# Performance work log

Measured on AMD Instinct MI355X. Metric: run time of the kernel, lower is better.

Reference implementation:

```python
import jax, jax.numpy as jnp
import numpy as np

F_SIZE = 1000   # feature_size
FIELDS = 39     # field_size
K = 40          # ffm embedding dim
BATCH = 4096
LAYERS = [1024, 512, 256]


def setup_inputs() -> dict:
    key = jax.random.key(0)
    ks = jax.random.split(key, 12)
    inp = {
        "X": jax.random.normal(ks[0], (BATCH, F_SIZE), dtype=jnp.float32),
        "w1": jax.random.normal(ks[1], (F_SIZE,), dtype=jnp.float32) * 0.01,
        "b": jnp.full((1,), 0.5, dtype=jnp.float32),
        "nfk": jax.random.normal(ks[2], (F_SIZE, FIELDS, K), dtype=jnp.float32) * 0.01,
        "f2f": jax.random.randint(ks[3], (F_SIZE,), 0, FIELDS, dtype=jnp.int32),
    }
    dims = [F_SIZE] + LAYERS
    for i in range(len(LAYERS)):
        fan_in, fan_out = dims[i], dims[i + 1]
        scale = np.sqrt(6.0 / (fan_in + fan_out)).astype(np.float32)
        inp[f"deepW{i}"] = jax.random.uniform(ks[4 + i], (fan_in, fan_out), dtype=jnp.float32, minval=-scale, maxval=scale)
        inp[f"deepB{i}"] = jnp.zeros((fan_out,), dtype=jnp.float32)
    scale = np.sqrt(6.0 / (LAYERS[-1] + 1)).astype(np.float32)
    inp["outW"] = jax.random.uniform(ks[10], (LAYERS[-1], 1), dtype=jnp.float32, minval=-scale, maxval=scale)
    inp["outB"] = jnp.zeros((1,), dtype=jnp.float32)
    return inp


def reference(X, w1, b, nfk, f2f, deepW0, deepB0, deepW1, deepB1, deepW2, deepB2, outW, outB):
    # --- linear term: sum_i w1[i]*X[:,i] + b ---
    linear = X @ w1 + b[0]                                  # [B]

    # --- field-aware interaction ---
    # A[i, j, :] = nfk[i, f2f[j], :]  (gather over fields)
    F = nfk.shape[0]
    A = nfk[jnp.arange(F)[:, None], f2f[None, :], :]        # [F, F, K]
    # S[i, j] = <nfk[i, f2f[j]], nfk[j, f2f[i]]> -- batch-independent scalar
    S = jnp.einsum('ijk,jik->ij', A, A)                     # [F, F]
    M = jnp.triu(S, 1)                                      # keep i < j pairs only
    # sum_{i<j} S[i,j] * X[:,i] * X[:,j]
    interaction = jnp.sum((X @ M) * X, axis=1)              # [B]

    # --- deep part (train=False: no dropout) ---
    h = jax.nn.relu(X @ deepW0 + deepB0)
    h = jax.nn.relu(h @ deepW1 + deepB1)
    h = jax.nn.relu(h @ deepW2 + deepB2)
    deep = (h @ outW + outB).reshape(-1)                    # [B]

    out_sum = linear + interaction + deep                   # logits [B]
    return out_sum
```

## Files before the change

### kernel.cpp

```cpp
#include <hip/hip_runtime.h>


#define BATCH   4096
#define FSZ     1000
#define NFIELDS 39
#define KDIM    40

typedef __attribute__((ext_vector_type(8))) short short8v;
typedef __attribute__((ext_vector_type(4))) float f32x4;

__device__ __forceinline__ short f2bf(float f) {
  unsigned u = __builtin_bit_cast(unsigned, f);
  u += 0x7fff + ((u >> 16) & 1);
  return (short)(u >> 16);
}
__device__ __forceinline__ float bf2f(unsigned short h) {
  unsigned u = (unsigned)h << 16;
  return __builtin_bit_cast(float, u);
}

typedef const __attribute__((address_space(1))) unsigned int* gas_ptr;
typedef __attribute__((address_space(3))) unsigned int* las_ptr;
__device__ __forceinline__ void gload16(const void* g, void* l) {
  __builtin_amdgcn_global_load_lds((gas_ptr)g, (las_ptr)l, 16, 0, 0);
}

__device__ __forceinline__ void transp32(
    const float* __restrict__ in, short* __restrict__ out, int idx, int nx,
    int K_in, int N_in, int Kpad, float (*t)[33], int tid)
{
  int n0 = (idx % nx) * 32, k0 = (idx / nx) * 32;
  int tx = tid & 31, ty = tid >> 5;
  #pragma unroll
  for (int i = 0; i < 32; i += 8) {
    int k = k0 + ty + i, n = n0 + tx;
    t[ty + i][tx] = (k < K_in && n < N_in) ? in[(size_t)k * N_in + n] : 0.f;
  }
  __syncthreads();
  #pragma unroll
  for (int i = 0; i < 32; i += 8) {
    int n = n0 + ty + i, k = k0 + tx;
    if (n < N_in && k < Kpad) out[(size_t)n * Kpad + k] = f2bf(t[tx][ty + i]);
  }
}

__global__ __launch_bounds__(256) void prep_kernel(
    const float* __restrict__ X, const float* __restrict__ nfk,
    const int* __restrict__ f2f,
    const float* __restrict__ W0, const float* __restrict__ W1,
    const float* __restrict__ W2,
    short* __restrict__ Xb, short* __restrict__ B12,
    short* __restrict__ Wt1, short* __restrict__ Wt2)
{
  __shared__ float tbuf[32][33];
  __shared__ float C[NFIELDS * 44];
  const int bid = blockIdx.x, tid = threadIdx.x;
  if (bid < 4096) {
    int k = tid * 4;
    short4 o = make_short4(0, 0, 0, 0);
    if (k < FSZ) {
      float4 v = *(const float4*)(X + (size_t)bid * FSZ + k);
      o = make_short4(f2bf(v.x), f2bf(v.y), f2bf(v.z), f2bf(v.w));
    }
    *(short4*)(Xb + (size_t)bid * 1024 + k) = o;
  } else if (bid < 5120) {
    int n = bid - 4096;
    if (n < FSZ) {
      for (int t = tid; t < NFIELDS * KDIM; t += 256)
        C[(t / KDIM) * 44 + (t % KDIM)] = nfk[(size_t)n * (NFIELDS * KDIM) + t];
    }
    __syncthreads();
    int fn = (n < FSZ) ? f2f[n] : 0;
    #pragma unroll
    for (int kk = 0; kk < 4; ++kk) {
      int k = kk * 256 + tid;
      float s = 0.f;
      if (n < FSZ && k < n) {
        int fk = f2f[k];
        const float4* p = (const float4*)(nfk + ((size_t)k * NFIELDS + fn) * KDIM);
        const float4* q = (const float4*)&C[fk * 44];
        #pragma unroll
        for (int t = 0; t < KDIM / 4; ++t) {
          float4 a = p[t], b = q[t];
          s += a.x * b.x + a.y * b.y + a.z * b.z + a.w * b.w;
        }
      }
      B12[(size_t)n * 1024 + k] = f2bf(s);
    }
  } else if (bid < 6144) {
    transp32(W0, B12 + 1024 * 1024, bid - 5120, 32, 1000, 1024, 1024, tbuf, tid);
  } else if (bid < 6656) {
    transp32(W1, Wt1, bid - 6144, 16, 1024, 512, 1024, tbuf, tid);
  } else {
    transp32(W2, Wt2, bid - 6656, 8, 512, 256, 512, tbuf, tid);
  }
}

template<int BM, int BN, int EPI>
__global__ __launch_bounds__(256) void gemm_mfma(
    const short* __restrict__ A, const short* __restrict__ Bt,
    const float* __restrict__ bias, void* __restrict__ Cout,
    int N, int K,
    const short* __restrict__ Xb, const float* __restrict__ w1,
    float* __restrict__ partial,
    const float* __restrict__ c1, const float* __restrict__ c2)
{
  constexpr int AM = BM / 32, AN = BN / 32;
  __shared__ __align__(16) short As[2][BM * 64];
  __shared__ __align__(16) short Bs[2][BN * 64];
  __shared__ float pbuf[2][BM];

  const int tid  = threadIdx.x;
  const int wid  = tid >> 6;
  const int lane = tid & 63;
  const int wr   = wid >> 1, wc = wid & 1;
  const int row0 = blockIdx.y * BM;
  const int col0 = blockIdx.x * BN;

  const int lr8   = lane >> 3;
  const int cbase = (lane & 7) * 16;

  f32x4 acc[AM][AN];
  #pragma unroll
  for (int m = 0; m < AM; ++m)
    #pragma unroll
    for (int n = 0; n < AN; ++n) acc[m][n] = (f32x4)(0.f);

  auto stage = [&](int p, int k0) {
    #pragma unroll
    for (int j = 0; j < BM / 32; ++j) {
      int i = j * 4 + wid;
      int r = i * 8 + lr8;
      int cb = cbase ^ ((r & 7) << 4);
      gload16((const char*)A + (((size_t)(row0 + r) * K + k0) << 1) + cb,
              (char*)&As[p][0] + i * 1024);
    }
    #pragma unroll
    for (int j = 0; j < BN / 32; ++j) {
      int i = j * 4 + wid;
      int r = i * 8 + lr8;
      int cb = cbase ^ ((r & 7) << 4);
      gload16((const char*)Bt + (((size_t)(col0 + r) * K + k0) << 1) + cb,
              (char*)&Bs[p][0] + i * 1024);
    }
  };

  auto compute = [&](int p) {
    #pragma unroll
    for (int kk = 0; kk < 2; ++kk) {
      const int cb = kk * 64 + (lane >> 4) * 16;
      short8v a[AM], b[AN];
      #pragma unroll
      for (int m = 0; m < AM; ++m) {
        int r = wr * (BM / 2) + m * 16 + (lane & 15);
        a[m] = *(const short8v*)((const char*)&As[p][0] + r * 128 + (cb ^ ((r & 7) << 4)));
      }
      #pragma unroll
      for (int n = 0; n < AN; ++n) {
        int r = wc * (BN / 2) + n * 16 + (lane & 15);
        b[n] = *(const short8v*)((const char*)&Bs[p][0] + r * 128 + (cb ^ ((r & 7) << 4)));
      }
      #pragma unroll
      for (int m = 0; m < AM; ++m)
        #pragma unroll
        for (int n = 0; n < AN; ++n)
          acc[m][n] = __builtin_amdgcn_mfma_f32_16x16x32_bf16(a[m], b[n], acc[m][n], 0, 0, 0);
    }
  };

  int nt = K >> 6;
  if (EPI == 0 && blockIdx.x < 8) {
    int need = ((int)blockIdx.x * 2) + 2;
    nt = nt < need ? nt : need;
  }

  stage(0, 0);
  __syncthreads();
  for (int t = 0; t < nt; ++t) {
    if (t + 1 < nt) stage((t + 1) & 1, (t + 1) << 6);
    compute(t & 1);
    __syncthreads();
  }

  const int cr = (lane >> 4) * 4;
  const int cc = lane & 15;

  if (EPI == 0) {
    if (blockIdx.x < 8) {
      float rsum[AM * 4];
      #pragma unroll
      for (int i = 0; i < AM * 4; ++i) rsum[i] = 0.f;
      #pragma unroll
      for (int m = 0; m < AM; ++m) {
        #pragma unroll
        for (int n = 0; n < AN; ++n) {
          int gc = col0 + wc * (BN / 2) + n * 16 + cc;
          float w1v = (gc < FSZ) ? w1[gc] : 0.f;
          #pragma unroll
          for (int r = 0; r < 4; ++r) {
            int gr = row0 + wr * (BM / 2) + m * 16 + cr + r;
            float xv = bf2f((unsigned short)Xb[(size_t)gr * 1024 + gc]);
            rsum[m * 4 + r] = fmaf(acc[m][n][r] + w1v, xv, rsum[m * 4 + r]);
          }
        }
      }
      #pragma unroll
      for (int mask = 1; mask < 16; mask <<= 1)
        #pragma unroll
        for (int i = 0; i < AM * 4; ++i)
          rsum[i] += __shfl_xor(rsum[i], mask, 64);
      if (cc == 0) {
        #pragma unroll
        for (int m = 0; m < AM; ++m)
          #pragma unroll
          for (int r = 0; r < 4; ++r)
            pbuf[wc][wr * (BM / 2) + m * 16 + cr + r] = rsum[m * 4 + r];
      }
      __syncthreads();
      if (tid < BM)
        partial[(size_t)(row0 + tid) * 8 + blockIdx.x] = pbuf[0][tid] + pbuf[1][tid];
    } else {
      #pragma unroll
      for (int m = 0; m < AM; ++m) {
        #pragma unroll
        for (int n = 0; n < AN; ++n) {
          int gc = col0 - 1024 + wc * (BN / 2) + n * 16 + cc;
          float bv = bias[gc];
          #pragma unroll
          for (int r = 0; r < 4; ++r) {
            int gr = row0 + wr * (BM / 2) + m * 16 + cr + r;
            float v = fmaxf(acc[m][n][r] + bv, 0.f);
            ((short*)Cout)[(size_t)gr * 1024 + gc] = f2bf(v);
          }
        }
      }
    }
  } else if (EPI == 1) {
    #pragma unroll
    for (int m = 0; m < AM; ++m) {
      #pragma unroll
      for (int n = 0; n < AN; ++n) {
        int gc = col0 + wc * (BN / 2) + n * 16 + cc;
        float bv = bias[gc];
        #pragma unroll
        for (int r = 0; r < 4; ++r) {
          int gr = row0 + wr * (BM / 2) + m * 16 + cr + r;
          float v = fmaxf(acc[m][n][r] + bv, 0.f);
          ((short*)Cout)[(size_t)gr * N + gc] = f2bf(v);
        }
      }
    }
  } else {
    float rsum[AM * 4];
    #pragma unroll
    for (int i = 0; i < AM * 4; ++i) rsum[i] = 0.f;
    #pragma unroll
    for (int m = 0; m < AM; ++m) {
      #pragma unroll
      for (int n = 0; n < AN; ++n) {
        int gc = col0 + wc * (BN / 2) + n * 16 + cc;
        float bv = bias[gc];
        float ow = w1[gc];
        #pragma unroll
        for (int r = 0; r < 4; ++r) {
          float v = fmaxf(acc[m][n][r] + bv, 0.f);
          rsum[m * 4 + r] = fmaf(v, ow, rsum[m * 4 + r]);
        }
      }
    }
    #pragma unroll
    for (int mask = 1; mask < 16; mask <<= 1)
      #pragma unroll
      for (int i = 0; i < AM * 4; ++i)
        rsum[i] += __shfl_xor(rsum[i], mask, 64);
    if (cc == 0) {
      #pragma unroll
      for (int m = 0; m < AM; ++m)
        #pragma unroll
        for (int r = 0; r < 4; ++r)
          pbuf[wc][wr * (BM / 2) + m * 16 + cr + r] = rsum[m * 4 + r];
    }
    __syncthreads();
    if (tid < BM) {
      int gr = row0 + tid;
      const float4* pp = (const float4*)(partial + (size_t)gr * 8);
      float4 u = pp[0], v = pp[1];
      ((float*)Cout)[gr] = pbuf[0][tid] + pbuf[1][tid]
          + u.x + u.y + u.z + u.w + v.x + v.y + v.z + v.w + c1[0] + c2[0];
    }
  }
}

extern "C" void kernel_launch(void* const* d_in, const int* in_sizes, int n_in,
                              void* d_out, int out_size, void* d_ws, size_t ws_size,
                              hipStream_t stream) {
  const float* X   = (const float*)d_in[0];
  const float* w1  = (const float*)d_in[1];
  const float* bsc = (const float*)d_in[2];
  const float* nfk = (const float*)d_in[3];
  const int*   f2f = (const int*)d_in[4];
  const float* W0  = (const float*)d_in[5];
  const float* B0  = (const float*)d_in[6];
  const float* W1  = (const float*)d_in[7];
  const float* B1  = (const float*)d_in[8];
  const float* W2  = (const float*)d_in[9];
  const float* B2  = (const float*)d_in[10];
  const float* oW  = (const float*)d_in[11];
  const float* oB  = (const float*)d_in[12];
  float* out = (float*)d_out;

  char* ws = (char*)d_ws;
  short* Xb   = (short*)(ws);
  short* B12  = (short*)(ws + 8388608);
  short* Wt1  = (short*)(ws + 12582912);
  short* Wt2  = (short*)(ws + 13631488);
  float* part = (float*)(ws + 13893632);
  short* h0   = (short*)(ws + 14680064);
  short* h1   = (short*)(ws + 23068672);

  prep_kernel<<<6784, 256, 0, stream>>>(X, nfk, f2f, W0, W1, W2,
                                        Xb, B12, Wt1, Wt2);
  gemm_mfma<128, 128, 0><<<dim3(16, 32), 256, 0, stream>>>(
      Xb, B12, B0, h0, 2048, 1024, Xb, w1, part, nullptr, nullptr);
  gemm_mfma<64, 64, 1><<<dim3(8, 64), 256, 0, stream>>>(
      h0, Wt1, B1, h1, 512, 1024, nullptr, nullptr, nullptr, nullptr, nullptr);
  gemm_mfma<32, 256, 3><<<dim3(1, 128), 256, 0, stream>>>(
      h1, Wt2, B2, out, 256, 512, nullptr, oW, part, bsc, oB);
}
```

Measured before the change: 77.89 us.

## Fuse prep and three GEMMs into one cooperative persistent kernel with grid syncs

Replaces four kernel launches with a single cooperative kernel of 512 blocks that strides over the prep work units, then runs each GEMM stage separated by grid-wide barriers, reusing one 64KB shared buffer. The last GEMM switches to single-buffered staging so its shared footprint fits. The aim is to remove launch gaps and inter-kernel drain between stages. The costs are grid-sync overhead, only 512 resident blocks doing the 6784 prep units, reduced occupancy from the 64KB static shared memory, and a serialized final stage. Falls back to the original launches if the cooperative launch fails.

```diff
diff --git a/kernel.cpp b/kernel.cpp
--- a/kernel.cpp
+++ b/kernel.cpp
@@ -1,4 +1,6 @@
 #include <hip/hip_runtime.h>
+#include <hip/hip_cooperative_groups.h>
+namespace cg = cooperative_groups;
 
 
 #define BATCH   4096
@@ -44,7 +46,8 @@
   }
 }
 
-__global__ __launch_bounds__(256) void prep_kernel(
+__device__ __forceinline__ void prep_unit(
+    int u, int tid, char* sm,
     const float* __restrict__ X, const float* __restrict__ nfk,
     const int* __restrict__ f2f,
     const float* __restrict__ W0, const float* __restrict__ W1,
@@ -52,19 +55,18 @@
     short* __restrict__ Xb, short* __restrict__ B12,
     short* __restrict__ Wt1, short* __restrict__ Wt2)
 {
-  __shared__ float tbuf[32][33];
-  __shared__ float C[NFIELDS * 44];
-  const int bid = blockIdx.x, tid = threadIdx.x;
-  if (bid < 4096) {
+  float (*tbuf)[33] = (float(*)[33])sm;
+  float* C = (float*)(sm + 4224);
+  if (u < 4096) {
     int k = tid * 4;
     short4 o = make_short4(0, 0, 0, 0);
     if (k < FSZ) {
-      float4 v = *(const float4*)(X + (size_t)bid * FSZ + k);
+      float4 v = *(const float4*)(X + (size_t)u * FSZ + k);
       o = make_short4(f2bf(v.x), f2bf(v.y), f2bf(v.z), f2bf(v.w));
     }
-    *(short4*)(Xb + (size_t)bid * 1024 + k) = o;
-  } else if (bid < 5120) {
-    int n = bid - 4096;
+    *(short4*)(Xb + (size_t)u * 1024 + k) = o;
+  } else if (u < 5120) {
+    int n = u - 4096;
     if (n < FSZ) {
       for (int t = tid; t < NFIELDS * KDIM; t += 256)
         C[(t / KDIM) * 44 + (t % KDIM)] = nfk[(size_t)n * (NFIELDS * KDIM) + t];
@@ -87,17 +89,18 @@
       }
       B12[(size_t)n * 1024 + k] = f2bf(s);
     }
-  } else if (bid < 6144) {
-    transp32(W0, B12 + 1024 * 1024, bid - 5120, 32, 1000, 1024, 1024, tbuf, tid);
-  } else if (bid < 6656) {
-    transp32(W1, Wt1, bid - 6144, 16, 1024, 512, 1024, tbuf, tid);
+  } else if (u < 6144) {
+    transp32(W0, B12 + 1024 * 1024, u - 5120, 32, 1000, 1024, 1024, tbuf, tid);
+  } else if (u < 6656) {
+    transp32(W1, Wt1, u - 6144, 16, 1024, 512, 1024, tbuf, tid);
   } else {
-    transp32(W2, Wt2, bid - 6656, 8, 512, 256, 512, tbuf, tid);
+    transp32(W2, Wt2, u - 6656, 8, 512, 256, 512, tbuf, tid);
   }
 }
 
 template<int BM, int BN, int EPI>
-__global__ __launch_bounds__(256) void gemm_mfma(
+__device__ __forceinline__ void gemm_body(
+    char* sm, int bx, int by,
     const short* __restrict__ A, const short* __restrict__ Bt,
     const float* __restrict__ bias, void* __restrict__ Cout,
     int N, int K,
@@ -106,17 +109,19 @@
     const float* __restrict__ c1, const float* __restrict__ c2)
 {
   constexpr int AM = BM / 32, AN = BN / 32;
-  __shared__ __align__(16) short As[2][BM * 64];
-  __shared__ __align__(16) short Bs[2][BN * 64];
-  __shared__ float pbuf[2][BM];
+  constexpr bool DB = (EPI != 3);
+  constexpr int ABUF = 128 * BM;
+  constexpr int BBUF = 128 * BN;
+  char* Asb = sm;
+  char* Bsb = sm + (DB ? 2 * ABUF : ABUF);
+  float (*pb)[BM] = (float(*)[BM])sm;
 
   const int tid  = threadIdx.x;
   const int wid  = tid >> 6;
   const int lane = tid & 63;
   const int wr   = wid >> 1, wc = wid & 1;
-  const int row0 = blockIdx.y * BM;
-  const int col0 = blockIdx.x * BN;
-
+  const int row0 = by * BM;
+  const int col0 = bx * BN;
   const int lr8   = lane >> 3;
   const int cbase = (lane & 7) * 16;
 
@@ -133,7 +138,7 @@
       int r = i * 8 + lr8;
       int cb = cbase ^ ((r & 7) << 4);
       gload16((const char*)A + (((size_t)(row0 + r) * K + k0) << 1) + cb,
-              (char*)&As[p][0] + i * 1024);
+              Asb + p * ABUF + i * 1024);
     }
     #pragma unroll
     for (int j = 0; j < BN / 32; ++j) {
@@ -141,7 +146,7 @@
       int r = i * 8 + lr8;
       int cb = cbase ^ ((r & 7) << 4);
       gload16((const char*)Bt + (((size_t)(col0 + r) * K + k0) << 1) + cb,
-              (char*)&Bs[p][0] + i * 1024);
+              Bsb + p * BBUF + i * 1024);
     }
   };
 
@@ -153,12 +158,12 @@
       #pragma unroll
       for (int m = 0; m < AM; ++m) {
         int r = wr * (BM / 2) + m * 16 + (lane & 15);
-        a[m] = *(const short8v*)((const char*)&As[p][0] + r * 128 + (cb ^ ((r & 7) << 4)));
+        a[m] = *(const short8v*)(Asb + p * ABUF + r * 128 + (cb ^ ((r & 7) << 4)));
       }
       #pragma unroll
       for (int n = 0; n < AN; ++n) {
         int r = wc * (BN / 2) + n * 16 + (lane & 15);
-        b[n] = *(const short8v*)((const char*)&Bs[p][0] + r * 128 + (cb ^ ((r & 7) << 4)));
+        b[n] = *(const short8v*)(Bsb + p * BBUF + r * 128 + (cb ^ ((r & 7) << 4)));
       }
       #pragma unroll
       for (int m = 0; m < AM; ++m)
@@ -169,16 +174,27 @@
   };
 
   int nt = K >> 6;
-  if (EPI == 0 && blockIdx.x < 8) {
-    int need = ((int)blockIdx.x * 2) + 2;
+  if (EPI == 0 && bx < 8) {
+    int need = bx * 2 + 2;
     nt = nt < need ? nt : need;
   }
 
-  stage(0, 0);
-  __syncthreads();
-  for (int t = 0; t < nt; ++t) {
-    if (t + 1 < nt) stage((t + 1) & 1, (t + 1) << 6);
-    compute(t & 1);
+  if constexpr (DB) {
+    stage(0, 0);
+    __syncthreads();
+    for (int t = 0; t < nt; ++t) {
+      if (t + 1 < nt) stage((t + 1) & 1, (t + 1) << 6);
+      compute(t & 1);
+      __syncthreads();
+    }
+  } else {
+    for (int t = 0; t < nt; ++t) {
+      __syncthreads();
+      stage(0, t << 6);
+      asm volatile("s_waitcnt vmcnt(0)" ::: "memory");
+      __syncthreads();
+      compute(0);
+    }
     __syncthreads();
   }
 
@@ -186,7 +202,7 @@
   const int cc = lane & 15;
 
   if (EPI == 0) {
-    if (blockIdx.x < 8) {
+    if (bx < 8) {
       float rsum[AM * 4];
       #pragma unroll
       for (int i = 0; i < AM * 4; ++i) rsum[i] = 0.f;
@@ -214,11 +230,11 @@
         for (int m = 0; m < AM; ++m)
           #pragma unroll
           for (int r = 0; r < 4; ++r)
-            pbuf[wc][wr * (BM / 2) + m * 16 + cr + r] = rsum[m * 4 + r];
+            pb[wc][wr * (BM / 2) + m * 16 + cr + r] = rsum[m * 4 + r];
       }
       __syncthreads();
       if (tid < BM)
-        partial[(size_t)(row0 + tid) * 8 + blockIdx.x] = pbuf[0][tid] + pbuf[1][tid];
+        partial[(size_t)(row0 + tid) * 8 + bx] = pb[0][tid] + pb[1][tid];
     } else {
       #pragma unroll
       for (int m = 0; m < AM; ++m) {
@@ -278,17 +294,67 @@
       for (int m = 0; m < AM; ++m)
         #pragma unroll
         for (int r = 0; r < 4; ++r)
-          pbuf[wc][wr * (BM / 2) + m * 16 + cr + r] = rsum[m * 4 + r];
+          pb[wc][wr * (BM / 2) + m * 16 + cr + r] = rsum[m * 4 + r];
     }
     __syncthreads();
     if (tid < BM) {
       int gr = row0 + tid;
       const float4* pp = (const float4*)(partial + (size_t)gr * 8);
       float4 u = pp[0], v = pp[1];
-      ((float*)Cout)[gr] = pbuf[0][tid] + pbuf[1][tid]
+      ((float*)Cout)[gr] = pb[0][tid] + pb[1][tid]
           + u.x + u.y + u.z + u.w + v.x + v.y + v.z + v.w + c1[0] + c2[0];
     }
   }
+}
+
+__global__ __launch_bounds__(256, 2) void fused_kernel(
+    const float* X, const float* w1, const float* bsc, const float* nfk,
+    const int* f2f, const float* W0, const float* B0, const float* W1,
+    const float* B1, const float* W2, const float* B2, const float* oW,
+    const float* oB, float* out,
+    short* Xb, short* B12, short* Wt1, short* Wt2,
+    float* part, short* h0, short* h1)
+{
+  __shared__ __align__(16) char smem[65536];
+  cg::grid_group grid = cg::this_grid();
+  const int bid = blockIdx.x, tid = threadIdx.x;
+
+  for (int u = bid; u < 6784; u += 512) {
+    prep_unit(u, tid, smem, X, nfk, f2f, W0, W1, W2, Xb, B12, Wt1, Wt2);
+    __syncthreads();
+  }
+  grid.sync();
+  gemm_body<128, 128, 0>(smem, bid & 15, bid >> 4, Xb, B12, B0, h0,
+                         2048, 1024, Xb, w1, part, nullptr, nullptr);
+  grid.sync();
+  gemm_body<64, 64, 1>(smem, bid & 7, bid >> 3, h0, Wt1, B1, h1,
+                       512, 1024, nullptr, nullptr, nullptr, nullptr, nullptr);
+  grid.sync();
+  if (bid < 128)
+    gemm_body<32, 256, 3>(smem, 0, bid, h1, Wt2, B2, out,
+                          256, 512, nullptr, oW, part, bsc, oB);
+}
+
+__global__ __launch_bounds__(256) void prep_kernel(
+    const float* X, const float* nfk, const int* f2f,
+    const float* W0, const float* W1, const float* W2,
+    short* Xb, short* B12, short* Wt1, short* Wt2)
+{
+  __shared__ __align__(16) char smem[11136];
+  prep_unit(blockIdx.x, threadIdx.x, smem, X, nfk, f2f, W0, W1, W2,
+            Xb, B12, Wt1, Wt2);
+}
+
+template<int BM, int BN, int EPI>
+__global__ __launch_bounds__(256) void gemm_mfma(
+    const short* A, const short* Bt, const float* bias, void* Cout,
+    int N, int K, const short* Xb, const float* w1, float* partial,
+    const float* c1, const float* c2)
+{
+  constexpr int SM = (EPI != 3) ? 256 * (BM + BN) : 128 * (BM + BN);
+  __shared__ __align__(16) char smem[SM];
+  gemm_body<BM, BN, EPI>(smem, blockIdx.x, blockIdx.y, A, Bt, bias, Cout,
+                         N, K, Xb, w1, partial, c1, c2);
 }
 
 extern "C" void kernel_launch(void* const* d_in, const int* in_sizes, int n_in,
@@ -318,12 +384,24 @@
   short* h0   = (short*)(ws + 14680064);
   short* h1   = (short*)(ws + 23068672);
 
-  prep_kernel<<<6784, 256, 0, stream>>>(X, nfk, f2f, W0, W1, W2,
-                                        Xb, B12, Wt1, Wt2);
-  gemm_mfma<128, 128, 0><<<dim3(16, 32), 256, 0, stream>>>(
-      Xb, B12, B0, h0, 2048, 1024, Xb, w1, part, nullptr, nullptr);
-  gemm_mfma<64, 64, 1><<<dim3(8, 64), 256, 0, stream>>>(
-      h0, Wt1, B1, h1, 512, 1024, nullptr, nullptr, nullptr, nullptr, nullptr);
-  gemm_mfma<32, 256, 3><<<dim3(1, 128), 256, 0, stream>>>(
-      h1, Wt2, B2, out, 256, 512, nullptr, oW, part, bsc, oB);
-}
+  void* args[] = {
+    (void*)&X, (void*)&w1, (void*)&bsc, (void*)&nfk, (void*)&f2f,
+    (void*)&W0, (void*)&B0, (void*)&W1, (void*)&B1, (void*)&W2, (void*)&B2,
+    (void*)&oW, (void*)&oB, (void*)&out,
+    (void*)&Xb, (void*)&B12, (void*)&Wt1, (void*)&Wt2,
+    (void*)&part, (void*)&h0, (void*)&h1 };
+
+  hipError_t err = hipLaunchCooperativeKernel(
+      (const void*)fused_kernel, dim3(512), dim3(256), args, 0, stream);
+
+  if (err != hipSuccess) {
+    prep_kernel<<<6784, 256, 0, stream>>>(X, nfk, f2f, W0, W1, W2,
+                                          Xb, B12, Wt1, Wt2);
+    gemm_mfma<128, 128, 0><<<dim3(16, 32), 256, 0, stream>>>(
+        Xb, B12, B0, h0, 2048, 1024, Xb, w1, part, nullptr, nullptr);
+    gemm_mfma<64, 64, 1><<<dim3(8, 64), 256, 0, stream>>>(
+        h0, Wt1, B1, h1, 512, 1024, nullptr, nullptr, nullptr, nullptr, nullptr);
+    gemm_mfma<32, 256, 3><<<dim3(1, 128), 256, 0, stream>>>(
+        h1, Wt2, B2, out, 256, 512, nullptr, oW, part, bsc, oB);
+  }
+}
```

Measured after the change: 265.6 us. 3.41x slower.

## Split prep kernel with field-major nfk copy and XCD-aware GEMM block swizzle

Applied to the files above, without the earlier changes.

The S-matrix computation is moved to a separate kernel that reads from a new field-major copy of nfk (nfkT[g][j][k]). With that layout, threads handling consecutive k load contiguous 160-byte rows instead of rows strided by 39*40 floats. The copy is built by extra blocks in the first prep kernel, which costs one more launch and roughly 6 MB of extra traffic. Separately, the GEMM kernels remap block indices so that blocks landing on the same XCD (lin&7) cover contiguous tiles, aiming for better L2 reuse.

```diff
diff --git a/kernel.cpp b/kernel.cpp
--- a/kernel.cpp
+++ b/kernel.cpp
@@ -44,16 +44,15 @@
   }
 }
 
-__global__ __launch_bounds__(256) void prep_kernel(
+__global__ __launch_bounds__(256) void prep_a_kernel(
     const float* __restrict__ X, const float* __restrict__ nfk,
-    const int* __restrict__ f2f,
     const float* __restrict__ W0, const float* __restrict__ W1,
     const float* __restrict__ W2,
     short* __restrict__ Xb, short* __restrict__ B12,
-    short* __restrict__ Wt1, short* __restrict__ Wt2)
+    short* __restrict__ Wt1, short* __restrict__ Wt2,
+    float* __restrict__ nfkT)
 {
   __shared__ float tbuf[32][33];
-  __shared__ float C[NFIELDS * 44];
   const int bid = blockIdx.x, tid = threadIdx.x;
   if (bid < 4096) {
     int k = tid * 4;
@@ -64,35 +63,52 @@
     }
     *(short4*)(Xb + (size_t)bid * 1024 + k) = o;
   } else if (bid < 5120) {
-    int n = bid - 4096;
-    if (n < FSZ) {
-      for (int t = tid; t < NFIELDS * KDIM; t += 256)
-        C[(t / KDIM) * 44 + (t % KDIM)] = nfk[(size_t)n * (NFIELDS * KDIM) + t];
-    }
-    __syncthreads();
-    int fn = (n < FSZ) ? f2f[n] : 0;
-    #pragma unroll
-    for (int kk = 0; kk < 4; ++kk) {
-      int k = kk * 256 + tid;
-      float s = 0.f;
-      if (n < FSZ && k < n) {
-        int fk = f2f[k];
-        const float4* p = (const float4*)(nfk + ((size_t)k * NFIELDS + fn) * KDIM);
-        const float4* q = (const float4*)&C[fk * 44];
-        #pragma unroll
-        for (int t = 0; t < KDIM / 4; ++t) {
-          float4 a = p[t], b = q[t];
-          s += a.x * b.x + a.y * b.y + a.z * b.z + a.w * b.w;
-        }
-      }
-      B12[(size_t)n * 1024 + k] = f2bf(s);
-    }
-  } else if (bid < 6144) {
-    transp32(W0, B12 + 1024 * 1024, bid - 5120, 32, 1000, 1024, 1024, tbuf, tid);
-  } else if (bid < 6656) {
-    transp32(W1, Wt1, bid - 6144, 16, 1024, 512, 1024, tbuf, tid);
+    transp32(W0, B12 + 1024 * 1024, bid - 4096, 32, 1000, 1024, 1024, tbuf, tid);
+  } else if (bid < 5632) {
+    transp32(W1, Wt1, bid - 5120, 16, 1024, 512, 1024, tbuf, tid);
+  } else if (bid < 5760) {
+    transp32(W2, Wt2, bid - 5632, 8, 512, 256, 512, tbuf, tid);
   } else {
-    transp32(W2, Wt2, bid - 6656, 8, 512, 256, 512, tbuf, tid);
+    int idx = bid - 5760;
+    int g = idx >> 2, jc = idx & 3;
+    int j = jc * 256 + tid;
+    if (j < FSZ && g < NFIELDS) {
+      const float4* src = (const float4*)(nfk + ((size_t)j * NFIELDS + g) * KDIM);
+      float4* dst = (float4*)(nfkT + ((size_t)g * FSZ + j) * KDIM);
+      #pragma unroll
+      for (int t = 0; t < KDIM / 4; ++t) dst[t] = src[t];
+    }
+  }
+}
+
+__global__ __launch_bounds__(256) void prep_b_kernel(
+    const float* __restrict__ nfk, const float* __restrict__ nfkT,
+    const int* __restrict__ f2f, short* __restrict__ B12)
+{
+  __shared__ float C[NFIELDS * 44];
+  const int n = blockIdx.x, tid = threadIdx.x;
+  if (n < FSZ) {
+    for (int t = tid; t < NFIELDS * KDIM; t += 256)
+      C[(t / KDIM) * 44 + (t % KDIM)] = nfk[(size_t)n * (NFIELDS * KDIM) + t];
+  }
+  __syncthreads();
+  int fn = (n < FSZ) ? f2f[n] : 0;
+  const float* pbase = nfkT + (size_t)fn * FSZ * KDIM;
+  #pragma unroll
+  for (int kk = 0; kk < 4; ++kk) {
+    int k = kk * 256 + tid;
+    float s = 0.f;
+    if (n < FSZ && k < n) {
+      int fk = f2f[k];
+      const float4* p = (const float4*)(pbase + (size_t)k * KDIM);
+      const float4* q = (const float4*)&C[fk * 44];
+      #pragma unroll
+      for (int t = 0; t < KDIM / 4; ++t) {
+        float4 a = p[t], b = q[t];
+        s += a.x * b.x + a.y * b.y + a.z * b.z + a.w * b.w;
+      }
+    }
+    B12[(size_t)n * 1024 + k] = f2bf(s);
   }
 }
 
@@ -110,12 +126,19 @@
   __shared__ __align__(16) short Bs[2][BN * 64];
   __shared__ float pbuf[2][BM];
 
+  const int nwgx = gridDim.x;
+  const int lin  = blockIdx.y * nwgx + blockIdx.x;
+  const int cpx  = (nwgx * gridDim.y) >> 3;
+  const int slin = (lin & 7) * cpx + (lin >> 3);
+  const int bx   = slin % nwgx;
+  const int by   = slin / nwgx;
+
   const int tid  = threadIdx.x;
   const int wid  = tid >> 6;
   const int lane = tid & 63;
   const int wr   = wid >> 1, wc = wid & 1;
-  const int row0 = blockIdx.y * BM;
-  const int col0 = blockIdx.x * BN;
+  const int row0 = by * BM;
+  const int col0 = bx * BN;
 
   const int lr8   = lane >> 3;
   const int cbase = (lane & 7) * 16;
@@ -169,8 +192,8 @@
   };
 
   int nt = K >> 6;
-  if (EPI == 0 && blockIdx.x < 8) {
-    int need = ((int)blockIdx.x * 2) + 2;
+  if (EPI == 0 && bx < 8) {
+    int need = bx * 2 + 2;
     nt = nt < need ? nt : need;
   }
 
@@ -186,7 +209,7 @@
   const int cc = lane & 15;
 
   if (EPI == 0) {
-    if (blockIdx.x < 8) {
+    if (bx < 8) {
       float rsum[AM * 4];
       #pragma unroll
       for (int i = 0; i < AM * 4; ++i) rsum[i] = 0.f;
@@ -218,7 +241,7 @@
       }
       __syncthreads();
       if (tid < BM)
-        partial[(size_t)(row0 + tid) * 8 + blockIdx.x] = pbuf[0][tid] + pbuf[1][tid];
+        partial[(size_t)(row0 + tid) * 8 + bx] = pbuf[0][tid] + pbuf[1][tid];
     } else {
       #pragma unroll
       for (int m = 0; m < AM; ++m) {
@@ -317,9 +340,11 @@
   float* part = (float*)(ws + 13893632);
   short* h0   = (short*)(ws + 14680064);
   short* h1   = (short*)(ws + 23068672);
-
-  prep_kernel<<<6784, 256, 0, stream>>>(X, nfk, f2f, W0, W1, W2,
-                                        Xb, B12, Wt1, Wt2);
+  float* nfkT = (float*)(ws + 27262976);
+
+  prep_a_kernel<<<5916, 256, 0, stream>>>(X, nfk, W0, W1, W2,
+                                          Xb, B12, Wt1, Wt2, nfkT);
+  prep_b_kernel<<<1024, 256, 0, stream>>>(nfk, nfkT, f2f, B12);
   gemm_mfma<128, 128, 0><<<dim3(16, 32), 256, 0, stream>>>(
       Xb, B12, B0, h0, 2048, 1024, Xb, w1, part, nullptr, nullptr);
   gemm_mfma<64, 64, 1><<<dim3(8, 64), 256, 0, stream>>>(
```

Result: faster. 73.90 us (-5.1%).
